# Performance work log

Hardware: AMD Instinct MI355X
Metric: run time of the kernel (lower is better)

The kernel has to match this reference:

```python
import jax, jax.numpy as jnp
import numpy as np

L, M, B = 32768, 8, 8192      # lines, max neighbors per line, blocks
LIN, BIN, H = 768, 768, 512   # line_in_dim, block_in_dim, hidden_size
NH, DH = 8, 512 // 8          # heads, head_dim
LN_EPS = 1e-5


def _ln(x, g, b):
    mu = jnp.mean(x, axis=-1, keepdims=True)
    var = jnp.mean(jnp.square(x - mu), axis=-1, keepdims=True)
    return (x - mu) * jax.lax.rsqrt(var + LN_EPS) * g + b


def setup_inputs() -> dict:
    key = jax.random.key(0)
    ks = jax.random.split(key, 12)
    w = lambda k, shape, fan: jax.random.normal(k, shape, jnp.float32) * (fan ** -0.5)
    return {
        'global_lines': jax.random.normal(ks[0], (L, LIN), jnp.float32),
        'block_reprs': jax.random.normal(ks[1], (B, BIN), jnp.float32),
        'Wq': w(ks[2], (H, LIN), LIN),            # q_proj (no bias)
        'Wkv': w(ks[3], (H, BIN), BIN),           # kv_proj (no bias)
        'qn_g': jnp.ones((H,), jnp.float32), 'qn_b': jnp.zeros((H,), jnp.float32),
        'kvn_g': jnp.ones((H,), jnp.float32), 'kvn_b': jnp.zeros((H,), jnp.float32),
        'in_proj_w': w(ks[4], (3 * H, H), H), 'in_proj_b': jnp.zeros((3 * H,), jnp.float32),
        'out_w': w(ks[5], (H, H), H), 'out_b': jnp.zeros((H,), jnp.float32),
        'p1_w': w(ks[6], (H, 2 * H), 2 * H), 'p1_b': jnp.zeros((H,), jnp.float32),
        'ln1_g': jnp.ones((H,), jnp.float32), 'ln1_b': jnp.zeros((H,), jnp.float32),
        'p2_w': w(ks[7], (H, H), H), 'p2_b': jnp.zeros((H,), jnp.float32),
        'ln2_g': jnp.ones((H,), jnp.float32), 'ln2_b': jnp.zeros((H,), jnp.float32),
        'head_w': w(ks[8], (1, H), H), 'head_b': jnp.zeros((1,), jnp.float32),
        'K_indices': jax.random.randint(ks[9], (L, M), 0, B, jnp.int32),
        'neighbor_counts': jnp.clip(jax.random.randint(ks[10], (L,), 0, M + 1, jnp.int32), 1, M),
    }


def reference(global_lines, block_reprs, Wq, Wkv, qn_g, qn_b, kvn_g, kvn_b,
              in_proj_w, in_proj_b, out_w, out_b,
              p1_w, p1_b, ln1_g, ln1_b, p2_w, p2_b, ln2_g, ln2_b,
              head_w, head_b, K_indices, neighbor_counts):
    # q = LN(q_proj(lines))                              [L, H]
    q = _ln(global_lines @ Wq.T, qn_g, qn_b)
    # gather neighbor block reprs, project, LN           [L, M, H]
    kv = _ln(block_reprs[K_indices] @ Wkv.T, kvn_g, kvn_b)
    pad = jnp.arange(M)[None, :] >= neighbor_counts[:, None]  # True = padded key

    # torch nn.MultiheadAttention with query length 1 per line
    wq_i, wk_i, wv_i = jnp.split(in_proj_w, 3, axis=0)
    bq_i, bk_i, bv_i = jnp.split(in_proj_b, 3, axis=0)
    qh = (q @ wq_i.T + bq_i).reshape(L, NH, DH)
    kh = (kv @ wk_i.T + bk_i).reshape(L, M, NH, DH)
    vh = (kv @ wv_i.T + bv_i).reshape(L, M, NH, DH)
    scores = jnp.einsum('lhd,lmhd->lhm', qh, kh) / np.float32(np.sqrt(DH))
    scores = jnp.where(pad[:, None, :], jnp.finfo(scores.dtype).min, scores)
    attn = jax.nn.softmax(scores, axis=-1)
    ctx = jnp.einsum('lhm,lmhd->lhd', attn, vh).reshape(L, H)
    attn_out = ctx @ out_w.T + out_b

    # line_proj: Linear(2H->H) + LN + GELU + residual(Linear + LN + GELU)
    x = jnp.concatenate([q, attn_out], axis=-1)
    x = jax.nn.gelu(_ln(x @ p1_w.T + p1_b, ln1_g, ln1_b), approximate=False)
    x = x + jax.nn.gelu(_ln(x @ p2_w.T + p2_b, ln2_g, ln2_b), approximate=False)
    logits = (x @ head_w.T + head_b)[:, 0]
    return jax.nn.sigmoid(logits)
```

## Files before the change

### kernel.cpp

```cpp
#include <hip/hip_runtime.h>
#include <math.h>


typedef unsigned short u16;
typedef unsigned int u32;
using bf16x8 = __attribute__((ext_vector_type(8))) __bf16;
using u16x8  = __attribute__((ext_vector_type(8))) u16;
using f32x4  = __attribute__((ext_vector_type(4))) float;

__device__ __forceinline__ u16 f2bf(float f) {
    u32 u = __builtin_bit_cast(u32, f);
    u32 r = u + 0x7fffu + ((u >> 16) & 1u);
    return (u16)(r >> 16);
}
__device__ __forceinline__ float bf2f(u16 h) {
    return __builtin_bit_cast(float, (u32)h << 16);
}
__device__ __forceinline__ float gelu_exact(float x) {
    return 0.5f * x * (1.0f + erff(x * 0.70710678118654752440f));
}

__device__ __forceinline__ float breduce1(float s0, float* sm) {
    #pragma unroll
    for (int off = 32; off > 0; off >>= 1) s0 += __shfl_down(s0, off);
    const int lane = threadIdx.x & 63, w = threadIdx.x >> 6;
    __syncthreads();
    if (lane == 0) sm[w] = s0;
    __syncthreads();
    return sm[0] + sm[1] + sm[2] + sm[3];
}

__global__ __launch_bounds__(256) void cvt_merged(
    const float* __restrict__ s0, u16* __restrict__ d0, int nq0,
    const float* __restrict__ s1, u16* __restrict__ d1)
{
    const int g = blockIdx.x * 256 + threadIdx.x;
    const float* s; u16* d; int q;
    if (g < nq0) { s = s0; d = d0; q = g; }
    else         { s = s1; d = d1; q = g - nq0; }
    const float4 v = *reinterpret_cast<const float4*>(s + q * 4);
    ushort4 o = make_ushort4(f2bf(v.x), f2bf(v.y), f2bf(v.z), f2bf(v.w));
    *reinterpret_cast<ushort4*>(d + q * 4) = o;
}

struct CvtJobs {
    const float* s[5];
    u16* d[5];
    int cum[6];
};
__global__ __launch_bounds__(256) void cvt_multi(CvtJobs j)
{
    const int g = blockIdx.x * 256 + threadIdx.x;
    if (g >= j.cum[5]) return;
    int seg = 0;
    #pragma unroll
    for (int k = 1; k < 5; ++k) seg += (g >= j.cum[k]);
    const int q = g - j.cum[seg];
    const float4 v = *reinterpret_cast<const float4*>(j.s[seg] + q * 4);
    ushort4 o = make_ushort4(f2bf(v.x), f2bf(v.y), f2bf(v.z), f2bf(v.w));
    *reinterpret_cast<ushort4*>(j.d[seg] + q * 4) = o;
}

__global__ __launch_bounds__(256) void fold_w2(
    const float* __restrict__ p1w, const float* __restrict__ outw,
    u16* __restrict__ p1cb)
{
    __shared__ float As[16][65];
    __shared__ float Bs[16][65];
    const int tx = threadIdx.x & 15, ty = threadIdx.x >> 4;
    const int i0 = blockIdx.y * 64, j0 = blockIdx.x * 64;
    const int lr = threadIdx.x >> 2;
    const int lc = (threadIdx.x & 3) * 4;
    const int kr = threadIdx.x >> 4;
    const int jc = (threadIdx.x & 15) * 4;
    float acc[4][4] = {};
    for (int k0 = 0; k0 < 512; k0 += 16) {
        const float4 av = *reinterpret_cast<const float4*>(
            p1w + (size_t)(i0 + lr) * 1024 + 512 + k0 + lc);
        As[lc + 0][lr] = av.x; As[lc + 1][lr] = av.y;
        As[lc + 2][lr] = av.z; As[lc + 3][lr] = av.w;
        const float4 bv = *reinterpret_cast<const float4*>(
            outw + (size_t)(k0 + kr) * 512 + j0 + jc);
        Bs[kr][jc + 0] = bv.x; Bs[kr][jc + 1] = bv.y;
        Bs[kr][jc + 2] = bv.z; Bs[kr][jc + 3] = bv.w;
        __syncthreads();
        #pragma unroll
        for (int kk = 0; kk < 16; ++kk) {
            float a[4], b[4];
            #pragma unroll
            for (int i = 0; i < 4; ++i) a[i] = As[kk][ty * 4 + i];
            #pragma unroll
            for (int jj = 0; jj < 4; ++jj) b[jj] = Bs[kk][tx * 4 + jj];
            #pragma unroll
            for (int i = 0; i < 4; ++i)
                #pragma unroll
                for (int jj = 0; jj < 4; ++jj)
                    acc[i][jj] = fmaf(a[i], b[jj], acc[i][jj]);
        }
        __syncthreads();
    }
    #pragma unroll
    for (int i = 0; i < 4; ++i)
        #pragma unroll
        for (int jj = 0; jj < 4; ++jj)
            p1cb[(size_t)(i0 + ty * 4 + i) * 1024 + 512 + j0 + tx * 4 + jj] =
                f2bf(acc[i][jj]);
}

__global__ __launch_bounds__(64) void fold_bias(
    const float* __restrict__ p1w, const float* __restrict__ outb,
    const float* __restrict__ p1b, float* __restrict__ bias2)
{
    const int i = blockIdx.x, lane = threadIdx.x;
    float s = 0.0f;
    #pragma unroll
    for (int k = lane; k < 512; k += 64)
        s += p1w[(size_t)i * 1024 + 512 + k] * outb[k];
    #pragma unroll
    for (int off = 32; off > 0; off >>= 1) s += __shfl_down(s, off);
    if (lane == 0) bias2[i] = s + p1b[i];
}

struct GemmJob {
    const u16* A1; const u16* A2; int K1; int K;
    const u16* W; const float* bias;
    u16* C; int N; float* stats;
    int nbx;
    int nwg;
};

template<int A_MODE, bool STATS>
__global__ __launch_bounds__(256) void gemm_bf16(
    GemmJob j0, GemmJob j1, int n0)
{
    __shared__ __bf16 As[2 * 64 * 32];
    __shared__ __bf16 Ws[2 * 128 * 32];
    const int tid = threadIdx.x;
    const int w = tid >> 6, lane = tid & 63;

    GemmJob jb;
    int orig;
    if ((int)blockIdx.x < n0) { jb = j0; orig = blockIdx.x; }
    else                      { jb = j1; orig = blockIdx.x - n0; }

    const u32 wgid = ((u32)orig & 7u) * ((u32)jb.nwg >> 3) + ((u32)orig >> 3);
    const int bx = (int)(wgid % (u32)jb.nbx);
    const int row0 = (int)(wgid / (u32)jb.nbx) * 64;
    const int col0 = bx * 128;
    const int K = jb.K, K1 = jb.K1, N = jb.N;

    const int wrow = (w >> 1) * 32, wcol = (w & 1) * 64;
    const int fr = lane & 15, fg = lane >> 4;
    const int fgx = fg ^ ((fr >> 1) & 3);

    int srow[2], scol[2], soff[2];
    #pragma unroll
    for (int c = 0; c < 2; ++c) {
        const int bo = w * 2048 + c * 1024 + lane * 16;
        srow[c] = bo >> 6;
        const int slot = (bo & 63) >> 4;
        scol[c] = (slot ^ ((srow[c] >> 1) & 3)) * 8;
        soff[c] = (w * 2048 + c * 1024) >> 1;
    }
    const int aoA = w * 1024 + lane * 16;
    const int srA = aoA >> 6;
    const int scA = (((aoA & 63) >> 4) ^ ((srA >> 1) & 3)) * 8;
    const int sofA = (w * 1024) >> 1;

    f32x4 acc[2][4] = {};

    auto stage_issue = [&](int k0, int buf) {
        const u16* asrc;
        if (A_MODE == 2 && k0 >= K1) {
            asrc = jb.A2 + (size_t)(row0 + srA) * (K - K1) + (k0 - K1) + scA;
        } else {
            const int ld = (A_MODE == 2) ? K1 : K;
            asrc = jb.A1 + (size_t)(row0 + srA) * ld + k0 + scA;
        }
        __builtin_amdgcn_global_load_lds(
            (const __attribute__((address_space(1))) u32*)asrc,
            (__attribute__((address_space(3))) u32*)(As + buf * 2048 + sofA),
            16, 0, 0);
        #pragma unroll
        for (int c = 0; c < 2; ++c) {
            const u16* wsrc = jb.W + (size_t)(col0 + srow[c]) * K + k0 + scol[c];
            __builtin_amdgcn_global_load_lds(
                (const __attribute__((address_space(1))) u32*)wsrc,
                (__attribute__((address_space(3))) u32*)(Ws + buf * 4096 + soff[c]),
                16, 0, 0);
        }
    };

    const int NT = K >> 5;

    stage_issue(0, 0);

    int bufc = 0;
    for (int t = 0; t < NT; ++t) {
        if (t + 1 < NT) {
            stage_issue((t + 1) << 5, bufc ^ 1);
            asm volatile("s_waitcnt vmcnt(3)" ::: "memory");
        } else {
            asm volatile("s_waitcnt vmcnt(0)" ::: "memory");
        }
        __builtin_amdgcn_s_barrier();
        __builtin_amdgcn_sched_barrier(0);

        bf16x8 af[2], bfr[4];
        #pragma unroll
        for (int m = 0; m < 2; ++m)
            af[m] = *(const bf16x8*)(As + bufc * 2048 + (wrow + m * 16 + fr) * 32 + fgx * 8);
        #pragma unroll
        for (int n = 0; n < 4; ++n)
            bfr[n] = *(const bf16x8*)(Ws + bufc * 4096 + (wcol + n * 16 + fr) * 32 + fgx * 8);
        #pragma unroll
        for (int m = 0; m < 2; ++m)
            #pragma unroll
            for (int n = 0; n < 4; ++n)
                acc[m][n] = __builtin_amdgcn_mfma_f32_16x16x32_bf16(
                    af[m], bfr[n], acc[m][n], 0, 0, 0);

        __builtin_amdgcn_s_barrier();
        bufc ^= 1;
    }

    if (jb.bias) {
        #pragma unroll
        for (int n = 0; n < 4; ++n) {
            const float bvv = jb.bias[col0 + wcol + n * 16 + fr];
            #pragma unroll
            for (int m = 0; m < 2; ++m)
                #pragma unroll
                for (int r = 0; r < 4; ++r)
                    acc[m][n][r] += bvv;
        }
    }

    #pragma unroll
    for (int m = 0; m < 2; ++m)
        #pragma unroll
        for (int n = 0; n < 4; ++n) {
            const int col = col0 + wcol + n * 16 + fr;
            #pragma unroll
            for (int r = 0; r < 4; ++r) {
                const int row = row0 + wrow + m * 16 + fg * 4 + r;
                jb.C[(size_t)row * N + col] = f2bf(acc[m][n][r]);
            }
        }

    if (STATS) {
        float ps[2][4], pq[2][4];
        #pragma unroll
        for (int m = 0; m < 2; ++m)
            #pragma unroll
            for (int r = 0; r < 4; ++r) {
                float s = 0.0f, q2 = 0.0f;
                #pragma unroll
                for (int n = 0; n < 4; ++n) {
                    const float v = acc[m][n][r];
                    s += v; q2 = fmaf(v, v, q2);
                }
                ps[m][r] = s; pq[m][r] = q2;
            }
        #pragma unroll
        for (int off = 1; off < 16; off <<= 1)
            #pragma unroll
            for (int m = 0; m < 2; ++m)
                #pragma unroll
                for (int r = 0; r < 4; ++r) {
                    ps[m][r] += __shfl_xor(ps[m][r], off);
                    pq[m][r] += __shfl_xor(pq[m][r], off);
                }
        if (fr == 0) {
            const int cb = bx * 2 + (w & 1);
            #pragma unroll
            for (int m = 0; m < 2; ++m)
                #pragma unroll
                for (int r = 0; r < 4; ++r) {
                    const int row = row0 + wrow + m * 16 + fg * 4 + r;
                    *reinterpret_cast<float2*>(jb.stats + ((size_t)row * 8 + cb) * 2) =
                        make_float2(ps[m][r], pq[m][r]);
                }
        }
    }
}

__global__ __launch_bounds__(256) void ln_merged(
    u16* __restrict__ X0, const float* __restrict__ st0,
    const float* __restrict__ g0, const float* __restrict__ b0, int n0,
    u16* __restrict__ X1, const float* __restrict__ st1,
    const float* __restrict__ g1, const float* __restrict__ b1)
{
    u16* X; const float* st; const float* g; const float* b; size_t row;
    if ((int)blockIdx.x < n0) { X = X0; st = st0; g = g0; b = b0; row = blockIdx.x; }
    else { X = X1; st = st1; g = g1; b = b1; row = blockIdx.x - n0; }
    float s = 0.0f, q2 = 0.0f;
    #pragma unroll
    for (int cb = 0; cb < 8; ++cb) {
        s  += st[(row * 8 + cb) * 2];
        q2 += st[(row * 8 + cb) * 2 + 1];
    }
    const float mu = s * (1.0f / 512.0f);
    const float var = q2 * (1.0f / 512.0f) - mu * mu;
    const float rs = rsqrtf(var + 1e-5f);
    const int t = threadIdx.x;
    const ushort2 xv = *reinterpret_cast<const ushort2*>(X + row * 512 + 2 * t);
    const float2 gg = *reinterpret_cast<const float2*>(g + 2 * t);
    const float2 bb = *reinterpret_cast<const float2*>(b + 2 * t);
    const float y0 = (bf2f(xv.x) - mu) * rs * gg.x + bb.x;
    const float y1 = (bf2f(xv.y) - mu) * rs * gg.y + bb.y;
    *reinterpret_cast<ushort2*>(X + row * 512 + 2 * t) = make_ushort2(f2bf(y0), f2bf(y1));
}

__global__ __launch_bounds__(256) void ln_rows_g(
    u16* __restrict__ X, const float* __restrict__ stats,
    const float* __restrict__ g, const float* __restrict__ b)
{
    const size_t row = blockIdx.x;
    float s = 0.0f, q2 = 0.0f;
    #pragma unroll
    for (int cb = 0; cb < 8; ++cb) {
        s  += stats[(row * 8 + cb) * 2];
        q2 += stats[(row * 8 + cb) * 2 + 1];
    }
    const float mu = s * (1.0f / 512.0f);
    const float var = q2 * (1.0f / 512.0f) - mu * mu;
    const float rs = rsqrtf(var + 1e-5f);
    const int t = threadIdx.x;
    const ushort2 xv = *reinterpret_cast<const ushort2*>(X + row * 512 + 2 * t);
    const float2 gg = *reinterpret_cast<const float2*>(g + 2 * t);
    const float2 bb = *reinterpret_cast<const float2*>(b + 2 * t);
    const float y0 = gelu_exact((bf2f(xv.x) - mu) * rs * gg.x + bb.x);
    const float y1 = gelu_exact((bf2f(xv.y) - mu) * rs * gg.y + bb.y);
    *reinterpret_cast<ushort2*>(X + row * 512 + 2 * t) = make_ushort2(f2bf(y0), f2bf(y1));
}

__global__ __launch_bounds__(512) void attn_kernel(
    const u16* __restrict__ qh, const u16* __restrict__ kvb,
    const int* __restrict__ kidx, const int* __restrict__ ncnt,
    u16* __restrict__ ctx)
{
    const int head = blockIdx.x & 7;
    const int grp  = blockIdx.x >> 3;
    const int ngrp = gridDim.x >> 3;
    const int wv   = threadIdx.x >> 6;
    const int lane = threadIdx.x & 63;
    const int mi = lane & 7, dg = lane >> 3;
    const bool b0 = (mi & 1), b1 = (mi & 2), b2 = (mi & 4);
    const int doff = (b0 ? 4 : 0) + (b1 ? 2 : 0) + (b2 ? 1 : 0);
    const int hoff = head * 64 + dg * 8;

    for (int l0 = (grp * 8 + wv) * 2; l0 < 32768; l0 += ngrp * 16) {
        int cnt[2], idxv[2];
        bool act[2];
        u16x8 qv[2], kv[2], vv[2];
        size_t kvbase[2];
        #pragma unroll
        for (int u = 0; u < 2; ++u) {
            const int l = l0 + u;
            cnt[u] = ncnt[l];
            idxv[u] = kidx[l * 8 + mi];
            act[u] = (mi < cnt[u]);
            kvbase[u] = (size_t)idxv[u] * 1024 + hoff;
            qv[u] = *(const u16x8*)(qh + (size_t)l * 512 + hoff);
            if (act[u]) {
                kv[u] = *(const u16x8*)(kvb + kvbase[u]);
                vv[u] = *(const u16x8*)(kvb + kvbase[u] + 512);
            }
        }

        float p[2] = {0.0f, 0.0f};
        #pragma unroll
        for (int u = 0; u < 2; ++u)
            if (act[u])
                #pragma unroll
                for (int jj = 0; jj < 8; ++jj)
                    p[u] = fmaf(bf2f(qv[u][jj]), bf2f(kv[u][jj]), p[u]);
        #pragma unroll
        for (int u = 0; u < 2; ++u) {
            p[u] += __shfl_xor(p[u], 8);
            p[u] += __shfl_xor(p[u], 16);
            p[u] += __shfl_xor(p[u], 32);
        }

        float s[2], mx[2], e[2], den[2], wgt[2];
        #pragma unroll
        for (int u = 0; u < 2; ++u) {
            s[u] = act[u] ? p[u] * 0.125f : -3.402823466e38f;
            mx[u] = s[u];
        }
        #pragma unroll
        for (int u = 0; u < 2; ++u) {
            mx[u] = fmaxf(mx[u], __shfl_xor(mx[u], 1));
            mx[u] = fmaxf(mx[u], __shfl_xor(mx[u], 2));
            mx[u] = fmaxf(mx[u], __shfl_xor(mx[u], 4));
        }
        #pragma unroll
        for (int u = 0; u < 2; ++u) { e[u] = __expf(s[u] - mx[u]); den[u] = e[u]; }
        #pragma unroll
        for (int u = 0; u < 2; ++u) {
            den[u] += __shfl_xor(den[u], 1);
            den[u] += __shfl_xor(den[u], 2);
            den[u] += __shfl_xor(den[u], 4);
        }
        #pragma unroll
        for (int u = 0; u < 2; ++u) wgt[u] = e[u] / den[u];

        float c[2][8] = {};
        #pragma unroll
        for (int u = 0; u < 2; ++u)
            if (act[u])
                #pragma unroll
                for (int jj = 0; jj < 8; ++jj)
                    c[u][jj] = wgt[u] * bf2f(vv[u][jj]);

        #pragma unroll
        for (int u = 0; u < 2; ++u)
            #pragma unroll
            for (int jj = 0; jj < 4; ++jj) {
                const float snd = b0 ? c[u][jj] : c[u][jj + 4];
                const float rec = __shfl_xor(snd, 1);
                c[u][jj] = (b0 ? c[u][jj + 4] : c[u][jj]) + rec;
            }
        #pragma unroll
        for (int u = 0; u < 2; ++u)
            #pragma unroll
            for (int jj = 0; jj < 2; ++jj) {
                const float snd = b1 ? c[u][jj] : c[u][jj + 2];
                const float rec = __shfl_xor(snd, 2);
                c[u][jj] = (b1 ? c[u][jj + 2] : c[u][jj]) + rec;
            }
        #pragma unroll
        for (int u = 0; u < 2; ++u) {
            const float snd = b2 ? c[u][0] : c[u][1];
            const float rec = __shfl_xor(snd, 4);
            c[u][0] = (b2 ? c[u][1] : c[u][0]) + rec;
        }
        #pragma unroll
        for (int u = 0; u < 2; ++u)
            ctx[(size_t)(l0 + u) * 512 + head * 64 + dg * 8 + doff] = f2bf(c[u][0]);
    }
}

__global__ __launch_bounds__(256) void final_head_s(
    const u16* __restrict__ h1, const u16* __restrict__ h2raw,
    const float* __restrict__ stats,
    const float* __restrict__ g, const float* __restrict__ b,
    const float* __restrict__ hw, const float* __restrict__ hb,
    float* __restrict__ out)
{
    __shared__ float sm[4];
    const size_t row = blockIdx.x;
    float s = 0.0f, q2 = 0.0f;
    #pragma unroll
    for (int cb = 0; cb < 8; ++cb) {
        s  += stats[(row * 8 + cb) * 2];
        q2 += stats[(row * 8 + cb) * 2 + 1];
    }
    const float mu = s * (1.0f / 512.0f);
    const float var = q2 * (1.0f / 512.0f) - mu * mu;
    const float rs = rsqrtf(var + 1e-5f);
    const int t = threadIdx.x;
    const ushort2 xv = *reinterpret_cast<const ushort2*>(h2raw + row * 512 + 2 * t);
    const ushort2 hv = *reinterpret_cast<const ushort2*>(h1 + row * 512 + 2 * t);
    const float2 gg = *reinterpret_cast<const float2*>(g + 2 * t);
    const float2 bb = *reinterpret_cast<const float2*>(b + 2 * t);
    const float2 hwv = *reinterpret_cast<const float2*>(hw + 2 * t);
    const float y0 = bf2f(hv.x) + gelu_exact((bf2f(xv.x) - mu) * rs * gg.x + bb.x);
    const float y1 = bf2f(hv.y) + gelu_exact((bf2f(xv.y) - mu) * rs * gg.y + bb.y);
    const float d = breduce1(y0 * hwv.x + y1 * hwv.y, sm);
    if (t == 0) out[row] = 1.0f / (1.0f + expf(-(d + hb[0])));
}

extern "C" void kernel_launch(void* const* d_in, const int* in_sizes, int n_in,
                              void* d_out, int out_size, void* d_ws, size_t ws_size,
                              hipStream_t stream)
{
    const float* lines  = (const float*)d_in[0];
    const float* blocks = (const float*)d_in[1];
    const float* Wq     = (const float*)d_in[2];
    const float* Wkv    = (const float*)d_in[3];
    const float* qn_g   = (const float*)d_in[4];
    const float* qn_b   = (const float*)d_in[5];
    const float* kvn_g  = (const float*)d_in[6];
    const float* kvn_b  = (const float*)d_in[7];
    const float* in_w   = (const float*)d_in[8];
    const float* in_b   = (const float*)d_in[9];
    const float* out_w  = (const float*)d_in[10];
    const float* out_b  = (const float*)d_in[11];
    const float* p1_w   = (const float*)d_in[12];
    const float* p1_b   = (const float*)d_in[13];
    const float* ln1_g  = (const float*)d_in[14];
    const float* ln1_b  = (const float*)d_in[15];
    const float* p2_w   = (const float*)d_in[16];
    const float* p2_b   = (const float*)d_in[17];
    const float* ln2_g  = (const float*)d_in[18];
    const float* ln2_b  = (const float*)d_in[19];
    const float* head_w = (const float*)d_in[20];
    const float* head_b = (const float*)d_in[21];
    const int*   kidx   = (const int*)d_in[22];
    const int*   ncnt   = (const int*)d_in[23];
    float* out = (float*)d_out;

    char* wsb = (char*)d_ws;
    u16* qb    = (u16*)(wsb);
    u16* qhb   = (u16*)(wsb + (32ull << 20));
    u16* Lb    = (u16*)(wsb + (32ull << 20));
    u16* ctxb  = (u16*)(wsb + (64ull << 20));
    u16* Bb    = (u16*)(wsb + (80ull << 20));
    u16* kvbb  = (u16*)(wsb + (96ull << 20));
    u16* bkvb  = (u16*)(wsb + (112ull << 20));
    float* stats_q   = (float*)(wsb + (120ull << 20));
    float* stats_h1  = (float*)(wsb + (124ull << 20));
    float* stats_h2  = (float*)(wsb + (128ull << 20));
    float* stats_bkv = (float*)(wsb + (132ull << 20));
    u16* Wqb   = (u16*)(wsb + (136ull << 20));
    u16* Wkvb  = Wqb + 512 * 768;
    u16* inwb  = Wkvb + 512 * 768;
    u16* p1cb  = inwb + 1536 * 512;
    u16* p2wb  = p1cb + 512 * 1024;
    float* bias2f = (float*)(p2wb + 512 * 512);

    {
        const int nq_lines = 32768 * 768 / 4;
        const int nq_blocks = 8192 * 768 / 4;
        cvt_merged<<<(nq_lines + nq_blocks) / 256, 256, 0, stream>>>(
            lines, Lb, nq_lines, blocks, Bb);
    }
    {
        CvtJobs j;
        const float* ss[5] = { Wq, Wkv, in_w, p1_w, p2_w };
        u16* dd[5] = { Wqb, Wkvb, inwb, p1cb, p2wb };
        const int nn[5] = { 512 * 768, 512 * 768, 1536 * 512, 512 * 1024, 512 * 512 };
        int c = 0;
        for (int k = 0; k < 5; ++k) { j.s[k] = ss[k]; j.d[k] = dd[k]; j.cum[k] = c; c += nn[k] / 4; }
        j.cum[5] = c;
        cvt_multi<<<(c + 255) / 256, 256, 0, stream>>>(j);
    }
    fold_w2<<<dim3(8, 8), 256, 0, stream>>>(p1_w, out_w, p1cb);
    fold_bias<<<512, 64, 0, stream>>>(p1_w, out_b, p1_b, bias2f);

    GemmJob JD = {};

    {
        GemmJob jq  = { Lb, nullptr, 768, 768, Wqb,  nullptr, qb,   512, stats_q,   4, 2048 };
        GemmJob jbk = { Bb, nullptr, 768, 768, Wkvb, nullptr, bkvb, 512, stats_bkv, 4, 512 };
        gemm_bf16<0, true><<<2560, 256, 0, stream>>>(jq, jbk, 2048);
    }
    ln_merged<<<32768 + 8192, 256, 0, stream>>>(
        qb, stats_q, qn_g, qn_b, 32768, bkvb, stats_bkv, kvn_g, kvn_b);
    {
        GemmJob jqh = { qb,   nullptr, 512, 512, inwb,             in_b,       qhb,  512,  nullptr, 4, 2048 };
        GemmJob jkv = { bkvb, nullptr, 512, 512, inwb + 512 * 512, in_b + 512, kvbb, 1024, nullptr, 8, 1024 };
        gemm_bf16<0, false><<<3072, 256, 0, stream>>>(jqh, jkv, 2048);
    }
    attn_kernel<<<2048, 512, 0, stream>>>(qhb, kvbb, kidx, ncnt, ctxb);
    {
        GemmJob jh1 = { qb, ctxb, 512, 1024, p1cb, bias2f, qhb, 512, stats_h1, 4, 2048 };
        gemm_bf16<2, true><<<2048, 256, 0, stream>>>(jh1, JD, 2048);
    }
    ln_rows_g<<<32768, 256, 0, stream>>>(qhb, stats_h1, ln1_g, ln1_b);
    {
        GemmJob jh2 = { qhb, nullptr, 512, 512, p2wb, p2_b, ctxb, 512, stats_h2, 4, 2048 };
        gemm_bf16<0, true><<<2048, 256, 0, stream>>>(jh2, JD, 2048);
    }
    final_head_s<<<32768, 256, 0, stream>>>(qhb, ctxb, stats_h2, ln2_g, ln2_b,
                                            head_w, head_b, out);
}
```

Measured before the change: 403.1 us.

## Fuse fp32-to-bf16 activation conversion into the first projection GEMM's A-tile load

After: 410.0 us. Within noise of the previous version (+1.7%).

```diff
diff --git a/kernel.cpp b/kernel.cpp
--- a/kernel.cpp
+++ b/kernel.cpp
@@ -28,19 +28,6 @@
     if (lane == 0) sm[w] = s0;
     __syncthreads();
     return sm[0] + sm[1] + sm[2] + sm[3];
-}
-
-__global__ __launch_bounds__(256) void cvt_merged(
-    const float* __restrict__ s0, u16* __restrict__ d0, int nq0,
-    const float* __restrict__ s1, u16* __restrict__ d1)
-{
-    const int g = blockIdx.x * 256 + threadIdx.x;
-    const float* s; u16* d; int q;
-    if (g < nq0) { s = s0; d = d0; q = g; }
-    else         { s = s1; d = d1; q = g - nq0; }
-    const float4 v = *reinterpret_cast<const float4*>(s + q * 4);
-    ushort4 o = make_ushort4(f2bf(v.x), f2bf(v.y), f2bf(v.z), f2bf(v.w));
-    *reinterpret_cast<ushort4*>(d + q * 4) = o;
 }
 
 struct CvtJobs {
@@ -122,7 +109,7 @@
 }
 
 struct GemmJob {
-    const u16* A1; const u16* A2; int K1; int K;
+    const u16* A1; const u16* A2; const float* A1f; int K1; int K;
     const u16* W; const float* bias;
     u16* C; int N; float* stats;
     int nbx;
@@ -166,21 +153,31 @@
     const int srA = aoA >> 6;
     const int scA = (((aoA & 63) >> 4) ^ ((srA >> 1) & 3)) * 8;
     const int sofA = (w * 1024) >> 1;
+    const int arF = tid >> 2;
+    const int acF = (tid & 3) * 8;
+    const int slotF = ((acF >> 3) ^ ((arF >> 1) & 3));
 
     f32x4 acc[2][4] = {};
+    float4 avlo, avhi;
 
     auto stage_issue = [&](int k0, int buf) {
-        const u16* asrc;
-        if (A_MODE == 2 && k0 >= K1) {
-            asrc = jb.A2 + (size_t)(row0 + srA) * (K - K1) + (k0 - K1) + scA;
+        if (A_MODE == 1) {
+            const float* src = jb.A1f + (size_t)(row0 + arF) * K + k0 + acF;
+            avlo = *reinterpret_cast<const float4*>(src);
+            avhi = *reinterpret_cast<const float4*>(src + 4);
         } else {
-            const int ld = (A_MODE == 2) ? K1 : K;
-            asrc = jb.A1 + (size_t)(row0 + srA) * ld + k0 + scA;
-        }
-        __builtin_amdgcn_global_load_lds(
-            (const __attribute__((address_space(1))) u32*)asrc,
-            (__attribute__((address_space(3))) u32*)(As + buf * 2048 + sofA),
-            16, 0, 0);
+            const u16* asrc;
+            if (A_MODE == 2 && k0 >= K1) {
+                asrc = jb.A2 + (size_t)(row0 + srA) * (K - K1) + (k0 - K1) + scA;
+            } else {
+                const int ld = (A_MODE == 2) ? K1 : K;
+                asrc = jb.A1 + (size_t)(row0 + srA) * ld + k0 + scA;
+            }
+            __builtin_amdgcn_global_load_lds(
+                (const __attribute__((address_space(1))) u32*)asrc,
+                (__attribute__((address_space(3))) u32*)(As + buf * 2048 + sofA),
+                16, 0, 0);
+        }
         #pragma unroll
         for (int c = 0; c < 2; ++c) {
             const u16* wsrc = jb.W + (size_t)(col0 + srow[c]) * K + k0 + scol[c];
@@ -190,16 +187,27 @@
                 16, 0, 0);
         }
     };
+    auto stage_write = [&](int buf) {
+        u16x8 o;
+        o[0] = f2bf(avlo.x); o[1] = f2bf(avlo.y); o[2] = f2bf(avlo.z); o[3] = f2bf(avlo.w);
+        o[4] = f2bf(avhi.x); o[5] = f2bf(avhi.y); o[6] = f2bf(avhi.z); o[7] = f2bf(avhi.w);
+        *reinterpret_cast<u16x8*>((u16*)As + buf * 2048 + arF * 32 + slotF * 8) = o;
+    };
 
     const int NT = K >> 5;
 
     stage_issue(0, 0);
+    if (A_MODE == 1) {
+        stage_write(0);
+        asm volatile("s_waitcnt lgkmcnt(0)" ::: "memory");
+    }
 
     int bufc = 0;
     for (int t = 0; t < NT; ++t) {
         if (t + 1 < NT) {
             stage_issue((t + 1) << 5, bufc ^ 1);
-            asm volatile("s_waitcnt vmcnt(3)" ::: "memory");
+            if (A_MODE == 1) asm volatile("s_waitcnt vmcnt(4)" ::: "memory");
+            else             asm volatile("s_waitcnt vmcnt(3)" ::: "memory");
         } else {
             asm volatile("s_waitcnt vmcnt(0)" ::: "memory");
         }
@@ -220,6 +228,10 @@
                 acc[m][n] = __builtin_amdgcn_mfma_f32_16x16x32_bf16(
                     af[m], bfr[n], acc[m][n], 0, 0, 0);
 
+        if (A_MODE == 1 && t + 1 < NT) {
+            stage_write(bufc ^ 1);
+            asm volatile("s_waitcnt lgkmcnt(0)" ::: "memory");
+        }
         __builtin_amdgcn_s_barrier();
         bufc ^= 1;
     }
@@ -505,9 +517,7 @@
     char* wsb = (char*)d_ws;
     u16* qb    = (u16*)(wsb);
     u16* qhb   = (u16*)(wsb + (32ull << 20));
-    u16* Lb    = (u16*)(wsb + (32ull << 20));
     u16* ctxb  = (u16*)(wsb + (64ull << 20));
-    u16* Bb    = (u16*)(wsb + (80ull << 20));
     u16* kvbb  = (u16*)(wsb + (96ull << 20));
     u16* bkvb  = (u16*)(wsb + (112ull << 20));
     float* stats_q   = (float*)(wsb + (120ull << 20));
@@ -522,12 +532,6 @@
     float* bias2f = (float*)(p2wb + 512 * 512);
 
     {
-        const int nq_lines = 32768 * 768 / 4;
-        const int nq_blocks = 8192 * 768 / 4;
-        cvt_merged<<<(nq_lines + nq_blocks) / 256, 256, 0, stream>>>(
-            lines, Lb, nq_lines, blocks, Bb);
-    }
-    {
         CvtJobs j;
         const float* ss[5] = { Wq, Wkv, in_w, p1_w, p2_w };
         u16* dd[5] = { Wqb, Wkvb, inwb, p1cb, p2wb };
@@ -543,25 +547,25 @@
     GemmJob JD = {};
 
     {
-        GemmJob jq  = { Lb, nullptr, 768, 768, Wqb,  nullptr, qb,   512, stats_q,   4, 2048 };
-        GemmJob jbk = { Bb, nullptr, 768, 768, Wkvb, nullptr, bkvb, 512, stats_bkv, 4, 512 };
-        gemm_bf16<0, true><<<2560, 256, 0, stream>>>(jq, jbk, 2048);
+        GemmJob jq  = { nullptr, nullptr, lines,  768, 768, Wqb,  nullptr, qb,   512, stats_q,   4, 2048 };
+        GemmJob jbk = { nullptr, nullptr, blocks, 768, 768, Wkvb, nullptr, bkvb, 512, stats_bkv, 4, 512 };
+        gemm_bf16<1, true><<<2560, 256, 0, stream>>>(jq, jbk, 2048);
     }
     ln_merged<<<32768 + 8192, 256, 0, stream>>>(
         qb, stats_q, qn_g, qn_b, 32768, bkvb, stats_bkv, kvn_g, kvn_b);
     {
-        GemmJob jqh = { qb,   nullptr, 512, 512, inwb,             in_b,       qhb,  512,  nullptr, 4, 2048 };
-        GemmJob jkv = { bkvb, nullptr, 512, 512, inwb + 512 * 512, in_b + 512, kvbb, 1024, nullptr, 8, 1024 };
+        GemmJob jqh = { qb,   nullptr, nullptr, 512, 512, inwb,             in_b,       qhb,  512,  nullptr, 4, 2048 };
+        GemmJob jkv = { bkvb, nullptr, nullptr, 512, 512, inwb + 512 * 512, in_b + 512, kvbb, 1024, nullptr, 8, 1024 };
         gemm_bf16<0, false><<<3072, 256, 0, stream>>>(jqh, jkv, 2048);
     }
     attn_kernel<<<2048, 512, 0, stream>>>(qhb, kvbb, kidx, ncnt, ctxb);
     {
-        GemmJob jh1 = { qb, ctxb, 512, 1024, p1cb, bias2f, qhb, 512, stats_h1, 4, 2048 };
+        GemmJob jh1 = { qb, ctxb, nullptr, 512, 1024, p1cb, bias2f, qhb, 512, stats_h1, 4, 2048 };
         gemm_bf16<2, true><<<2048, 256, 0, stream>>>(jh1, JD, 2048);
     }
     ln_rows_g<<<32768, 256, 0, stream>>>(qhb, stats_h1, ln1_g, ln1_b);
     {
-        GemmJob jh2 = { qhb, nullptr, 512, 512, p2wb, p2_b, ctxb, 512, stats_h2, 4, 2048 };
+        GemmJob jh2 = { qhb, nullptr, nullptr, 512, 512, p2wb, p2_b, ctxb, 512, stats_h2, 4, 2048 };
         gemm_bf16<0, true><<<2048, 256, 0, stream>>>(jh2, JD, 2048);
     }
     final_head_s<<<32768, 256, 0, stream>>>(qhb, ctxb, stats_h2, ln2_g, ln2_b,
```
